# Performance work log

Hardware: AMD Instinct MI355X
Metric: run time of the kernel (lower is better)

Reference implementation:

```python
import jax, jax.numpy as jnp
import numpy as np

HIDDEN = 1024
N_HEADS = 16
HEAD_DIM = HIDDEN // N_HEADS


def apply_rope(x, freqs):
    # x: [b, s, h, d]; freqs: [s, d//2]
    b, s, h, d = x.shape
    x2 = x.reshape(b, s, h, d // 2, 2)
    x_real, x_imag = x2[..., 0], x2[..., 1]
    cos = jnp.cos(freqs)[None, :, None, :]  # [1, s, 1, d//2]
    sin = jnp.sin(freqs)[None, :, None, :]
    out_real = x_real * cos - x_imag * sin
    out_imag = x_real * sin + x_imag * cos
    return jnp.stack([out_real, out_imag], axis=-1).reshape(b, s, h, d)


def setup_inputs() -> dict:
    key = jax.random.key(0)
    k_x, k_f, k_wq, k_bq, k_wo, k_bo = jax.random.split(key, 6)
    b, s = 2, 2048
    x = jax.random.normal(k_x, (b, s, HIDDEN), dtype=jnp.float32)
    freqs = jax.random.normal(k_f, (s, HEAD_DIM // 2), dtype=jnp.float32)
    lim = 1.0 / np.sqrt(HIDDEN)
    W_qkv = jax.random.uniform(k_wq, (HIDDEN, 3 * HIDDEN), jnp.float32, -lim, lim)
    b_qkv = jax.random.uniform(k_bq, (3 * HIDDEN,), jnp.float32, -lim, lim)
    W_out = jax.random.uniform(k_wo, (HIDDEN, HIDDEN), jnp.float32, -lim, lim)
    b_out = jax.random.uniform(k_bo, (HIDDEN,), jnp.float32, -lim, lim)
    return {"x": x, "freqs": freqs, "W_qkv": W_qkv, "b_qkv": b_qkv,
            "W_out": W_out, "b_out": b_out}


def reference(x, freqs, W_qkv, b_qkv, W_out, b_out):
    b, s, c = x.shape
    h, d = N_HEADS, HEAD_DIM
    qkv = jnp.einsum('bsc,cf->bsf', x, W_qkv) + b_qkv  # [b, s, 3*c]
    qkv = qkv.reshape(b, s, 3, h, d)
    q, k, v = qkv[:, :, 0], qkv[:, :, 1], qkv[:, :, 2]  # [b, s, h, d]
    q = apply_rope(q, freqs)
    k = apply_rope(k, freqs)
    scale = 1.0 / np.sqrt(d).astype(np.float32)
    scores = jnp.einsum('bqhd,bkhd->bhqk', q, k) * scale  # [b, h, s, s]
    attn = jax.nn.softmax(scores, axis=-1)
    out = jnp.einsum('bhqk,bkhd->bqhd', attn, v).reshape(b, s, c)
    return jnp.einsum('bsc,cf->bsf', out, W_out) + b_out
```

## Files before the change

kernel.cpp:

```cpp
#include <hip/hip_runtime.h>
#include <math.h>

constexpr int kB = 2;
constexpr int kS = 2048;
constexpr int kC = 1024;
constexpr int kH = 16;
constexpr int kD = 64;
constexpr int kF = 3072;
constexpr int kT = kB * kS;

typedef __attribute__((ext_vector_type(8))) short short8v;
typedef __attribute__((ext_vector_type(4))) short short4v;
typedef __attribute__((ext_vector_type(4))) float f32x4;
typedef __attribute__((ext_vector_type(16))) float f32x16;

__device__ __forceinline__ short f2bf(float f) {
    unsigned u = __builtin_bit_cast(unsigned, f);
    u += 0x7fffu + ((u >> 16) & 1u);
    return (short)(u >> 16);
}

__device__ __forceinline__ unsigned cvtpk(float a, float b) {
    unsigned r;
    asm("v_cvt_pk_bf16_f32 %0, %1, %2" : "=v"(r) : "v"(a), "v"(b));
    return r;
}

__device__ __forceinline__ unsigned pk_bf16(float a, float b) {
    unsigned ua = __builtin_bit_cast(unsigned, a);
    ua += 0x7fffu + ((ua >> 16) & 1u);
    unsigned ub = __builtin_bit_cast(unsigned, b);
    ub += 0x7fffu + ((ub >> 16) & 1u);
    return (ua >> 16) | (ub & 0xffff0000u);
}

__device__ __forceinline__ void gl_lds16(const void* g, void* l) {
    __builtin_amdgcn_global_load_lds(
        (const __attribute__((address_space(1))) char*)g,
        (__attribute__((address_space(3))) char*)l, 16, 0, 0);
}

__device__ __forceinline__ f32x4 mfma16(short8v a, short8v b, f32x4 c) {
    return __builtin_amdgcn_mfma_f32_16x16x32_bf16(a, b, c, 0, 0, 0);
}
__device__ __forceinline__ f32x16 mfma32(short8v a, short8v b, f32x16 c) {
    return __builtin_amdgcn_mfma_f32_32x32x16_bf16(a, b, c, 0, 0, 0);
}

__device__ __forceinline__ void tcvt_body(const float* __restrict__ w,
                                          short* __restrict__ wt, int K, int N,
                                          int bx, int by, int t, float Ts[64][65]) {
    const int n0 = bx * 64, k0 = by * 64;
    const int r = t >> 4, c4 = (t & 15) * 4;
#pragma unroll
    for (int rr = 0; rr < 64; rr += 16) {
        float4 v = *reinterpret_cast<const float4*>(&w[(size_t)(k0 + r + rr) * N + n0 + c4]);
        Ts[r + rr][c4 + 0] = v.x; Ts[r + rr][c4 + 1] = v.y;
        Ts[r + rr][c4 + 2] = v.z; Ts[r + rr][c4 + 3] = v.w;
    }
    __syncthreads();
#pragma unroll
    for (int rr = 0; rr < 64; rr += 16) {
        int n = r + rr;
        short4v o = { f2bf(Ts[c4 + 0][n]), f2bf(Ts[c4 + 1][n]),
                      f2bf(Ts[c4 + 2][n]), f2bf(Ts[c4 + 3][n]) };
        *reinterpret_cast<short4v*>(&wt[(size_t)(n0 + n) * K + k0 + c4]) = o;
    }
}

__global__ __launch_bounds__(256) void prep_kernel(
    const float* __restrict__ x, short* __restrict__ xb,
    const float* __restrict__ wq, short* __restrict__ wqt,
    const float* __restrict__ wo, short* __restrict__ wot,
    const float* __restrict__ freqs, float* __restrict__ cost,
    float* __restrict__ sint) {
    __shared__ float Ts[64][65];
    const int bid = blockIdx.x, t = threadIdx.x;
    if (bid < 4096) {
        int i = bid * 256 + t;
        float4 v = reinterpret_cast<const float4*>(x)[i];
        short4v o = { f2bf(v.x), f2bf(v.y), f2bf(v.z), f2bf(v.w) };
        reinterpret_cast<short4v*>(xb)[i] = o;
    } else if (bid < 4864) {
        int i = bid - 4096;
        tcvt_body(wq, wqt, kC, kF, i % 48, i / 48, t, Ts);
    } else if (bid < 5120) {
        int i = bid - 4864;
        tcvt_body(wo, wot, kC, kC, i % 16, i / 16, t, Ts);
    } else {
        int i = (bid - 5120) * 256 + t;
        float f = freqs[i];
        float s, c;
        sincosf(f, &s, &c);
        cost[i] = c; sint[i] = s;
    }
}

__device__ __forceinline__ void gemm_main(const short* __restrict__ A,
                                          const short* __restrict__ Bt,
                                          int m0, int n0, short* Als, short* Bls,
                                          f32x4 acc[4][4]) {
    const int tid = threadIdx.x, wid = tid >> 6, lane = tid & 63;
    const int srow = lane >> 3, schunk = lane & 7;
    const int fr = lane & 15, fg = lane >> 4;
    const int wm = (wid >> 1) * 64, wn = (wid & 1) * 64;
    for (int kt = 0; kt < 1024; kt += 64) {
        __syncthreads();
#pragma unroll
        for (int j = 0; j < 4; ++j) {
            int i = wid * 4 + j;
            int row = i * 8 + srow;
            gl_lds16(&A[(size_t)(m0 + row) * 1024 + kt + ((schunk ^ (row & 7)) << 3)],
                     &Als[i * 512]);
        }
#pragma unroll
        for (int j = 0; j < 4; ++j) {
            int i = wid * 4 + j;
            int row = i * 8 + srow;
            gl_lds16(&Bt[(size_t)(n0 + row) * 1024 + kt + ((schunk ^ (row & 7)) << 3)],
                     &Bls[i * 512]);
        }
        __syncthreads();
#pragma unroll
        for (int kk = 0; kk < 2; ++kk) {
            short8v af[4], bf[4];
#pragma unroll
            for (int fm = 0; fm < 4; ++fm) {
                int row = wm + fm * 16 + fr;
                af[fm] = *reinterpret_cast<const short8v*>(
                    &Als[row * 64 + (((fg + 4 * kk) ^ (row & 7)) << 3)]);
            }
#pragma unroll
            for (int fn = 0; fn < 4; ++fn) {
                int row = wn + fn * 16 + fr;
                bf[fn] = *reinterpret_cast<const short8v*>(
                    &Bls[row * 64 + (((fg + 4 * kk) ^ (row & 7)) << 3)]);
            }
#pragma unroll
            for (int fm = 0; fm < 4; ++fm)
#pragma unroll
                for (int fn = 0; fn < 4; ++fn)
                    acc[fm][fn] = mfma16(af[fm], bf[fn], acc[fm][fn]);
        }
    }
}

__global__ __launch_bounds__(256) void qkv_gemm_kernel(
    const short* __restrict__ xb, const short* __restrict__ wqt,
    const float* __restrict__ bias, const float* __restrict__ cost,
    const float* __restrict__ sint,
    short* __restrict__ qg, short* __restrict__ kg, short* __restrict__ vt) {
    __shared__ __attribute__((aligned(16))) short Als[128 * 64];
    __shared__ __attribute__((aligned(16))) short Bls[128 * 64];
    f32x4 acc[4][4] = {};
    const int tid = threadIdx.x, wid = tid >> 6, lane = tid & 63;
    const int m0 = blockIdx.y * 128, n0 = blockIdx.x * 128;
    gemm_main(xb, wqt, m0, n0, Als, Bls, acc);

    const int fr = lane & 15, fg = lane >> 4;
    const int wm = (wid >> 1) * 64, wn = (wid & 1) * 64;
    const int which = (n0 + wn) >> 10;
    const int bidx = m0 >> 11;
#pragma unroll
    for (int fn = 0; fn < 4; ++fn) {
        int col = n0 + wn + fn * 16 + fr;
        float bv = bias[col];
        int d = col & 63;
        int h = (col >> 6) & 15;
        int p0 = d >> 1;
        int odd = d & 1;
#pragma unroll
        for (int fm = 0; fm < 4; ++fm) {
            int r0 = m0 + wm + fm * 16 + fg * 4;
            int s0 = r0 & 2047;
            float c[4];
#pragma unroll
            for (int r = 0; r < 4; ++r) c[r] = acc[fm][fn][r] + bv;
            if (which < 2) {
#pragma unroll
                for (int r = 0; r < 4; ++r) {
                    float cs = cost[(s0 + r) * 32 + p0];
                    float sn = sint[(s0 + r) * 32 + p0];
                    float p = __shfl_xor(c[r], 1);
                    float o = odd ? fmaf(p, sn, c[r] * cs) : fmaf(-p, sn, c[r] * cs);
                    c[r] = (which == 0) ? o * 0.1803368801f : o;
                }
                short* dst = which ? kg : qg;
                size_t base = ((size_t)(bidx * 16 + h) * 2048 + s0) * 64 + d;
#pragma unroll
                for (int r = 0; r < 4; ++r) dst[base + (size_t)r * 64] = f2bf(c[r]);
            } else {
                short4v o = { f2bf(c[0]), f2bf(c[1]), f2bf(c[2]), f2bf(c[3]) };
                *reinterpret_cast<short4v*>(
                    &vt[((size_t)(bidx * 16 + h) * 64 + d) * 2048 + s0]) = o;
            }
        }
    }
}

__global__ __launch_bounds__(256, 3) void attn_mfma_kernel(
    const short* __restrict__ qg, const short* __restrict__ kg,
    const short* __restrict__ vt, short* __restrict__ ab) {
    __shared__ __attribute__((aligned(16))) short LDSBUF[3 * 8192];
    const int tid = threadIdx.x, wid = tid >> 6, lane = tid & 63;
    const int l31 = lane & 31, hi = lane >> 5;
    const int p = wid >> 1;
    const int wq = wid & 1;
    const int r8 = lane >> 3, c8 = lane & 7;
    const int soff = 8 * (c8 ^ r8);

    const int bid = blockIdx.x;
    const int swz = (bid & 7) * 128 + (bid >> 3);
    const int bh = swz >> 5;
    const int q0 = (swz & 31) * 64 + wq * 32;

    const short* qb = qg + (size_t)bh * 2048 * 64;
    const short* kb = kg + (size_t)bh * 2048 * 64;
    const short* vb = vt + (size_t)bh * 64 * 2048;

    short8v qf[4];
#pragma unroll
    for (int kkq = 0; kkq < 4; ++kkq)
        qf[kkq] = *reinterpret_cast<const short8v*>(
            &qb[(size_t)(q0 + l31) * 64 + kkq * 16 + hi * 8]);

    f32x16 o[2] = {};
    float l_i = 0.f;

    auto stage = [&](int t, short* buf) {
        const int kt = t * 32;
        short* Kd = buf + p * 2048 + (wq * 8) * 64;
        const short* Ks = kb + (size_t)(p * 1024 + kt) * 64;
#pragma unroll
        for (int j = 0; j < 2; ++j) {
            int row = j * 16 + wq * 8 + r8;
            gl_lds16(Ks + (size_t)row * 64 + soff, Kd + j * 1024);
        }
        short* Vd = buf + 4096 + (wid * 8) * 64;
        const int s = c8 ^ r8;
#pragma unroll
        for (int j = 0; j < 2; ++j) {
            int d = j * 32 + wid * 8 + r8;
            gl_lds16(vb + (size_t)d * 2048 + (s >> 2) * 1024 + kt + (s & 3) * 8,
                     Vd + j * 2048);
        }
    };

    stage(0, LDSBUF);
    stage(1, LDSBUF + 8192);

    for (int t = 0; t < 32; ++t) {
        __builtin_amdgcn_sched_barrier(0);
        if (t < 31) {
            asm volatile("s_waitcnt vmcnt(4)" ::: "memory");
        } else {
            asm volatile("s_waitcnt vmcnt(0)" ::: "memory");
        }
        __builtin_amdgcn_s_barrier();
        __builtin_amdgcn_sched_barrier(0);

        short* bufc = LDSBUF + (t % 3) * 8192;
        if (t + 2 < 32) stage(t + 2, LDSBUF + ((t + 2) % 3) * 8192);

        const short* Kb = bufc + p * 2048;
        const short* Vb = bufc + 4096;

        f32x16 sacc = {};
#pragma unroll
        for (int kkq = 0; kkq < 4; ++kkq) {
            short8v a = *reinterpret_cast<const short8v*>(
                &Kb[l31 * 64 + (((kkq * 2 + hi) ^ (l31 & 7)) << 3)]);
            sacc = mfma32(a, qf[kkq], sacc);
        }

#pragma unroll
        for (int r = 0; r < 16; ++r) sacc[r] = __builtin_amdgcn_exp2f(sacc[r]);
        float t8[8];
#pragma unroll
        for (int r = 0; r < 8; ++r) t8[r] = sacc[r] + sacc[r + 8];
        float t4[4];
#pragma unroll
        for (int r = 0; r < 4; ++r) t4[r] = t8[r] + t8[r + 4];
        float rs = (t4[0] + t4[1]) + (t4[2] + t4[3]);
        rs += __shfl_xor(rs, 32);
        l_i += rs;

        unsigned c[8];
#pragma unroll
        for (int i = 0; i < 8; ++i) c[i] = cvtpk(sacc[2 * i], sacc[2 * i + 1]);
        short8v pb[2];
#pragma unroll
        for (int kk = 0; kk < 2; ++kk) {
            unsigned a0 = c[kk * 4 + 0], a1 = c[kk * 4 + 1];
            unsigned a2 = c[kk * 4 + 2], a3 = c[kk * 4 + 3];
            unsigned s0x = (unsigned)__shfl_xor((int)a0, 32);
            unsigned s1x = (unsigned)__shfl_xor((int)a1, 32);
            unsigned s2x = (unsigned)__shfl_xor((int)a2, 32);
            unsigned s3x = (unsigned)__shfl_xor((int)a3, 32);
            uint4 w;
            w.x = hi ? s2x : a0;
            w.y = hi ? s3x : a1;
            w.z = hi ? a2 : s0x;
            w.w = hi ? a3 : s1x;
            pb[kk] = __builtin_bit_cast(short8v, w);
        }

#pragma unroll
        for (int kk = 0; kk < 2; ++kk) {
            short8v v0 = *reinterpret_cast<const short8v*>(
                &Vb[l31 * 64 + (((p * 4 + kk * 2 + hi) ^ (l31 & 7)) << 3)]);
            short8v v1 = *reinterpret_cast<const short8v*>(
                &Vb[(32 + l31) * 64 + (((p * 4 + kk * 2 + hi) ^ (l31 & 7)) << 3)]);
            o[0] = mfma32(v0, pb[kk], o[0]);
            o[1] = mfma32(v1, pb[kk], o[1]);
        }
    }

    __syncthreads();

    float* olds = reinterpret_cast<float*>(LDSBUF + 4096);
    float* lls  = olds + 2 * 2304;
    if (p == 1) {
        float* ob = olds + wq * 2304 + lane * 36;
#pragma unroll
        for (int i = 0; i < 4; ++i) {
            f32x4 w0 = { o[0][4 * i + 0], o[0][4 * i + 1], o[0][4 * i + 2], o[0][4 * i + 3] };
            *reinterpret_cast<f32x4*>(ob + i * 4) = w0;
            f32x4 w1 = { o[1][4 * i + 0], o[1][4 * i + 1], o[1][4 * i + 2], o[1][4 * i + 3] };
            *reinterpret_cast<f32x4*>(ob + 16 + i * 4) = w1;
        }
        lls[wq * 64 + lane] = l_i;
    }
    __syncthreads();
    if (p == 0) {
        float* ob = olds + wq * 2304 + lane * 36;
#pragma unroll
        for (int i = 0; i < 4; ++i) {
            f32x4 w0 = *reinterpret_cast<const f32x4*>(ob + i * 4);
            f32x4 w1 = *reinterpret_cast<const f32x4*>(ob + 16 + i * 4);
#pragma unroll
            for (int j = 0; j < 4; ++j) {
                o[0][4 * i + j] += w0[j];
                o[1][4 * i + j] += w1[j];
            }
        }
        l_i += lls[wq * 64 + lane];

        const float inv = 1.f / l_i;
        short* ep = LDSBUF + wid * 2048;
        const int q = l31;
#pragma unroll
        for (int fd = 0; fd < 2; ++fd)
#pragma unroll
            for (int i = 0; i < 4; ++i) {
                int d0 = fd * 32 + 8 * i + 4 * hi;
                uint2 w;
                w.x = pk_bf16(o[fd][4 * i + 0] * inv, o[fd][4 * i + 1] * inv);
                w.y = pk_bf16(o[fd][4 * i + 2] * inv, o[fd][4 * i + 3] * inv);
                *reinterpret_cast<uint2*>(&ep[q * 64 + (d0 ^ (8 * (q & 3)))]) = w;
            }
        __builtin_amdgcn_s_waitcnt(0);
        const int bb = bh >> 4, hh = bh & 15;
        const int wrow = r8, wcol = c8;
#pragma unroll
        for (int j = 0; j < 4; ++j) {
            int row = j * 8 + wrow;
            short8v tv = *reinterpret_cast<const short8v*>(
                &ep[row * 64 + ((8 * wcol) ^ (8 * (row & 3)))]);
            int s = q0 + row;
            *reinterpret_cast<short8v*>(
                &ab[(size_t)(bb * 2048 + s) * 1024 + hh * 64 + 8 * wcol]) = tv;
        }
    }
}

__global__ __launch_bounds__(256) void out_gemm_kernel(
    const short* __restrict__ ab, const short* __restrict__ wot,
    const float* __restrict__ bias, float* __restrict__ out) {
    __shared__ __attribute__((aligned(16))) short Als[128 * 64];
    __shared__ __attribute__((aligned(16))) short Bls[128 * 64];
    f32x4 acc[4][4] = {};
    const int tid = threadIdx.x, wid = tid >> 6, lane = tid & 63;
    const int m0 = blockIdx.y * 128, n0 = blockIdx.x * 128;
    gemm_main(ab, wot, m0, n0, Als, Bls, acc);
    const int fr = lane & 15, fg = lane >> 4;
    const int wm = (wid >> 1) * 64, wn = (wid & 1) * 64;
#pragma unroll
    for (int fn = 0; fn < 4; ++fn) {
        int col = n0 + wn + fn * 16 + fr;
        float bv = bias[col];
#pragma unroll
        for (int fm = 0; fm < 4; ++fm) {
            int r0 = m0 + wm + fm * 16 + fg * 4;
#pragma unroll
            for (int r = 0; r < 4; ++r)
                out[(size_t)(r0 + r) * 1024 + col] = acc[fm][fn][r] + bv;
        }
    }
}

extern "C" void kernel_launch(void* const* d_in, const int* in_sizes, int n_in,
                              void* d_out, int out_size, void* d_ws, size_t ws_size,
                              hipStream_t stream) {
    const float* x     = (const float*)d_in[0];
    const float* freqs = (const float*)d_in[1];
    const float* W_qkv = (const float*)d_in[2];
    const float* b_qkv = (const float*)d_in[3];
    const float* W_out = (const float*)d_in[4];
    const float* b_out = (const float*)d_in[5];
    float* out = (float*)d_out;

    char* w = (char*)d_ws;
    short* xb  = (short*)w;  w += (size_t)kT * kC * 2;
    short* wqt = (short*)w;  w += (size_t)kF * kC * 2;
    short* wot = (short*)w;  w += (size_t)kC * kC * 2;
    short* qgw = (short*)w;  w += (size_t)kB * kH * kS * kD * 2;
    short* kgw = (short*)w;  w += (size_t)kB * kH * kS * kD * 2;
    short* vtw = (short*)w;  w += (size_t)kB * kH * kS * kD * 2;
    short* abw = (short*)w;  w += (size_t)kT * kC * 2;
    float* costt = (float*)w; w += (size_t)kS * (kD / 2) * 4;
    float* sintt = (float*)w; w += (size_t)kS * (kD / 2) * 4;

    prep_kernel<<<dim3(5376), 256, 0, stream>>>(x, xb, W_qkv, wqt, W_out, wot,
                                                freqs, costt, sintt);
    qkv_gemm_kernel<<<dim3(kF / 128, kT / 128), 256, 0, stream>>>(
        xb, wqt, b_qkv, costt, sintt, qgw, kgw, vtw);
    attn_mfma_kernel<<<dim3(1024), 256, 0, stream>>>(qgw, kgw, vtw, abw);
    out_gemm_kernel<<<dim3(kC / 128, kT / 128), 256, 0, stream>>>(abw, wot, b_out, out);
}
```

Before: 137.0 us.

## Restructure attention kernel: each wave covers 64 queries over a key quarter

```diff
diff --git a/kernel.cpp b/kernel.cpp
--- a/kernel.cpp
+++ b/kernel.cpp
@@ -24,6 +24,10 @@
     unsigned r;
     asm("v_cvt_pk_bf16_f32 %0, %1, %2" : "=v"(r) : "v"(a), "v"(b));
     return r;
+}
+
+__device__ __forceinline__ void plane32_swap(unsigned& a, unsigned& b) {
+    asm volatile("v_permlane32_swap_b32 %0, %1" : "+v"(a), "+v"(b));
 }
 
 __device__ __forceinline__ unsigned pk_bf16(float a, float b) {
@@ -201,176 +205,148 @@
 __global__ __launch_bounds__(256, 3) void attn_mfma_kernel(
     const short* __restrict__ qg, const short* __restrict__ kg,
     const short* __restrict__ vt, short* __restrict__ ab) {
-    __shared__ __attribute__((aligned(16))) short LDSBUF[3 * 8192];
+    __shared__ __attribute__((aligned(16))) short LDSBUF[16384];
+    short* Kls = LDSBUF;
+    short* Vls = LDSBUF + 8192;
     const int tid = threadIdx.x, wid = tid >> 6, lane = tid & 63;
     const int l31 = lane & 31, hi = lane >> 5;
-    const int p = wid >> 1;
-    const int wq = wid & 1;
     const int r8 = lane >> 3, c8 = lane & 7;
-    const int soff = 8 * (c8 ^ r8);
 
     const int bid = blockIdx.x;
     const int swz = (bid & 7) * 128 + (bid >> 3);
     const int bh = swz >> 5;
-    const int q0 = (swz & 31) * 64 + wq * 32;
+    const int q0 = (swz & 31) * 64;
 
     const short* qb = qg + (size_t)bh * 2048 * 64;
     const short* kb = kg + (size_t)bh * 2048 * 64;
     const short* vb = vt + (size_t)bh * 64 * 2048;
 
-    short8v qf[4];
-#pragma unroll
-    for (int kkq = 0; kkq < 4; ++kkq)
-        qf[kkq] = *reinterpret_cast<const short8v*>(
-            &qb[(size_t)(q0 + l31) * 64 + kkq * 16 + hi * 8]);
-
-    f32x16 o[2] = {};
-    float l_i = 0.f;
-
-    auto stage = [&](int t, short* buf) {
-        const int kt = t * 32;
-        short* Kd = buf + p * 2048 + (wq * 8) * 64;
-        const short* Ks = kb + (size_t)(p * 1024 + kt) * 64;
-#pragma unroll
-        for (int j = 0; j < 2; ++j) {
-            int row = j * 16 + wq * 8 + r8;
-            gl_lds16(Ks + (size_t)row * 64 + soff, Kd + j * 1024);
-        }
-        short* Vd = buf + 4096 + (wid * 8) * 64;
-        const int s = c8 ^ r8;
-#pragma unroll
-        for (int j = 0; j < 2; ++j) {
-            int d = j * 32 + wid * 8 + r8;
-            gl_lds16(vb + (size_t)d * 2048 + (s >> 2) * 1024 + kt + (s & 3) * 8,
-                     Vd + j * 2048);
-        }
-    };
-
-    stage(0, LDSBUF);
-    stage(1, LDSBUF + 8192);
-
-    for (int t = 0; t < 32; ++t) {
-        __builtin_amdgcn_sched_barrier(0);
-        if (t < 31) {
-            asm volatile("s_waitcnt vmcnt(4)" ::: "memory");
-        } else {
-            asm volatile("s_waitcnt vmcnt(0)" ::: "memory");
-        }
-        __builtin_amdgcn_s_barrier();
-        __builtin_amdgcn_sched_barrier(0);
-
-        short* bufc = LDSBUF + (t % 3) * 8192;
-        if (t + 2 < 32) stage(t + 2, LDSBUF + ((t + 2) % 3) * 8192);
-
-        const short* Kb = bufc + p * 2048;
-        const short* Vb = bufc + 4096;
-
-        f32x16 sacc = {};
+    short8v qf[2][4];
+#pragma unroll
+    for (int qt = 0; qt < 2; ++qt)
+#pragma unroll
+        for (int kkq = 0; kkq < 4; ++kkq)
+            qf[qt][kkq] = *reinterpret_cast<const short8v*>(
+                &qb[(size_t)(q0 + qt * 32 + l31) * 64 + kkq * 16 + hi * 8]);
+
+    f32x16 o[2][2] = {};
+    float l_loc[2] = {0.f, 0.f};
+
+    const int soffK = 8 * (c8 ^ r8);
+
+    for (int t = 0; t < 16; ++t) {
+        const int kt = t * 128;
+        __syncthreads();
+#pragma unroll
+        for (int j = 0; j < 4; ++j)
+            gl_lds16(kb + (size_t)(kt + wid * 32 + j * 8 + r8) * 64 + soffK,
+                     Kls + (wid * 32 + j * 8) * 64);
+#pragma unroll
+        for (int j = 0; j < 4; ++j) {
+            int d = wid * 16 + j * 4 + (lane >> 4);
+            int c = lane & 15;
+            gl_lds16(vb + (size_t)d * 2048 + kt + ((c ^ (d & 15)) * 8),
+                     Vls + (wid * 16 + j * 4) * 128);
+        }
+        __syncthreads();
+
+        f32x16 sacc[2] = {};
 #pragma unroll
         for (int kkq = 0; kkq < 4; ++kkq) {
-            short8v a = *reinterpret_cast<const short8v*>(
-                &Kb[l31 * 64 + (((kkq * 2 + hi) ^ (l31 & 7)) << 3)]);
-            sacc = mfma32(a, qf[kkq], sacc);
-        }
-
-#pragma unroll
-        for (int r = 0; r < 16; ++r) sacc[r] = __builtin_amdgcn_exp2f(sacc[r]);
-        float t8[8];
-#pragma unroll
-        for (int r = 0; r < 8; ++r) t8[r] = sacc[r] + sacc[r + 8];
-        float t4[4];
-#pragma unroll
-        for (int r = 0; r < 4; ++r) t4[r] = t8[r] + t8[r + 4];
-        float rs = (t4[0] + t4[1]) + (t4[2] + t4[3]);
-        rs += __shfl_xor(rs, 32);
-        l_i += rs;
-
-        unsigned c[8];
-#pragma unroll
-        for (int i = 0; i < 8; ++i) c[i] = cvtpk(sacc[2 * i], sacc[2 * i + 1]);
-        short8v pb[2];
-#pragma unroll
-        for (int kk = 0; kk < 2; ++kk) {
-            unsigned a0 = c[kk * 4 + 0], a1 = c[kk * 4 + 1];
-            unsigned a2 = c[kk * 4 + 2], a3 = c[kk * 4 + 3];
-            unsigned s0x = (unsigned)__shfl_xor((int)a0, 32);
-            unsigned s1x = (unsigned)__shfl_xor((int)a1, 32);
-            unsigned s2x = (unsigned)__shfl_xor((int)a2, 32);
-            unsigned s3x = (unsigned)__shfl_xor((int)a3, 32);
-            uint4 w;
-            w.x = hi ? s2x : a0;
-            w.y = hi ? s3x : a1;
-            w.z = hi ? a2 : s0x;
-            w.w = hi ? a3 : s1x;
-            pb[kk] = __builtin_bit_cast(short8v, w);
-        }
-
-#pragma unroll
-        for (int kk = 0; kk < 2; ++kk) {
-            short8v v0 = *reinterpret_cast<const short8v*>(
-                &Vb[l31 * 64 + (((p * 4 + kk * 2 + hi) ^ (l31 & 7)) << 3)]);
-            short8v v1 = *reinterpret_cast<const short8v*>(
-                &Vb[(32 + l31) * 64 + (((p * 4 + kk * 2 + hi) ^ (l31 & 7)) << 3)]);
-            o[0] = mfma32(v0, pb[kk], o[0]);
-            o[1] = mfma32(v1, pb[kk], o[1]);
-        }
+            short8v kf = *reinterpret_cast<const short8v*>(
+                &Kls[(wid * 32 + l31) * 64 + (((kkq * 2 + hi) ^ (l31 & 7)) << 3)]);
+            sacc[0] = mfma32(kf, qf[0][kkq], sacc[0]);
+            sacc[1] = mfma32(kf, qf[1][kkq], sacc[1]);
+        }
+
+        short8v pb[2][2];
+#pragma unroll
+        for (int qt = 0; qt < 2; ++qt) {
+#pragma unroll
+            for (int r = 0; r < 16; ++r)
+                sacc[qt][r] = __builtin_amdgcn_exp2f(sacc[qt][r]);
+            float t8[8];
+#pragma unroll
+            for (int r = 0; r < 8; ++r) t8[r] = sacc[qt][r] + sacc[qt][r + 8];
+            float t4[4];
+#pragma unroll
+            for (int r = 0; r < 4; ++r) t4[r] = t8[r] + t8[r + 4];
+            l_loc[qt] += (t4[0] + t4[1]) + (t4[2] + t4[3]);
+            unsigned c[4][2];
+#pragma unroll
+            for (int g = 0; g < 4; ++g) {
+                c[g][0] = cvtpk(sacc[qt][g * 4 + 0], sacc[qt][g * 4 + 1]);
+                c[g][1] = cvtpk(sacc[qt][g * 4 + 2], sacc[qt][g * 4 + 3]);
+            }
+#pragma unroll
+            for (int kk = 0; kk < 2; ++kk) {
+                unsigned x0 = c[2 * kk][0], y0 = c[2 * kk + 1][0];
+                unsigned x1 = c[2 * kk][1], y1 = c[2 * kk + 1][1];
+                plane32_swap(x0, y0);
+                plane32_swap(x1, y1);
+                uint4 w;
+                w.x = x0; w.y = x1; w.z = y0; w.w = y1;
+                pb[qt][kk] = __builtin_bit_cast(short8v, w);
+            }
+        }
+
+#pragma unroll
+        for (int kk = 0; kk < 2; ++kk)
+#pragma unroll
+            for (int fd = 0; fd < 2; ++fd) {
+                int d = fd * 32 + l31;
+                short8v vf = *reinterpret_cast<const short8v*>(
+                    &Vls[d * 128 + (((wid * 4 + kk * 2 + hi) ^ (d & 15)) << 3)]);
+                o[fd][0] = mfma32(vf, pb[0][kk], o[fd][0]);
+                o[fd][1] = mfma32(vf, pb[1][kk], o[fd][1]);
+            }
     }
 
     __syncthreads();
 
-    float* olds = reinterpret_cast<float*>(LDSBUF + 4096);
-    float* lls  = olds + 2 * 2304;
-    if (p == 1) {
-        float* ob = olds + wq * 2304 + lane * 36;
-#pragma unroll
-        for (int i = 0; i < 4; ++i) {
-            f32x4 w0 = { o[0][4 * i + 0], o[0][4 * i + 1], o[0][4 * i + 2], o[0][4 * i + 3] };
-            *reinterpret_cast<f32x4*>(ob + i * 4) = w0;
-            f32x4 w1 = { o[1][4 * i + 0], o[1][4 * i + 1], o[1][4 * i + 2], o[1][4 * i + 3] };
-            *reinterpret_cast<f32x4*>(ob + 16 + i * 4) = w1;
-        }
-        lls[wq * 64 + lane] = l_i;
-    }
-    __syncthreads();
-    if (p == 0) {
-        float* ob = olds + wq * 2304 + lane * 36;
-#pragma unroll
-        for (int i = 0; i < 4; ++i) {
-            f32x4 w0 = *reinterpret_cast<const f32x4*>(ob + i * 4);
-            f32x4 w1 = *reinterpret_cast<const f32x4*>(ob + 16 + i * 4);
-#pragma unroll
-            for (int j = 0; j < 4; ++j) {
-                o[0][4 * i + j] += w0[j];
-                o[1][4 * i + j] += w1[j];
-            }
-        }
-        l_i += lls[wq * 64 + lane];
-
-        const float inv = 1.f / l_i;
-        short* ep = LDSBUF + wid * 2048;
-        const int q = l31;
-#pragma unroll
-        for (int fd = 0; fd < 2; ++fd)
-#pragma unroll
-            for (int i = 0; i < 4; ++i) {
-                int d0 = fd * 32 + 8 * i + 4 * hi;
-                uint2 w;
-                w.x = pk_bf16(o[fd][4 * i + 0] * inv, o[fd][4 * i + 1] * inv);
-                w.y = pk_bf16(o[fd][4 * i + 2] * inv, o[fd][4 * i + 3] * inv);
-                *reinterpret_cast<uint2*>(&ep[q * 64 + (d0 ^ (8 * (q & 3)))]) = w;
-            }
-        __builtin_amdgcn_s_waitcnt(0);
+    float* Oacc = reinterpret_cast<float*>(LDSBUF);
+    float* lacc = Oacc + 64 * 65;
+    float l2[2];
+#pragma unroll
+    for (int qt = 0; qt < 2; ++qt)
+        l2[qt] = l_loc[qt] + __shfl_xor(l_loc[qt], 32);
+    for (int w = 0; w < 4; ++w) {
+        if (wid == w) {
+#pragma unroll
+            for (int qt = 0; qt < 2; ++qt) {
+                int q = qt * 32 + l31;
+#pragma unroll
+                for (int fd = 0; fd < 2; ++fd)
+#pragma unroll
+                    for (int r = 0; r < 16; ++r) {
+                        int d = fd * 32 + (r & 3) + 8 * (r >> 2) + 4 * hi;
+                        if (w == 0) Oacc[q * 65 + d] = o[fd][qt][r];
+                        else        Oacc[q * 65 + d] += o[fd][qt][r];
+                    }
+                if (hi == 0) {
+                    if (w == 0) lacc[q] = l2[qt];
+                    else        lacc[q] += l2[qt];
+                }
+            }
+        }
+        __syncthreads();
+    }
+    {
+        const int q = tid >> 2, dc = (tid & 3) * 16;
+        const float inv = 1.f / lacc[q];
+        unsigned u[8];
+#pragma unroll
+        for (int i = 0; i < 8; ++i) {
+            float a = Oacc[q * 65 + dc + 2 * i] * inv;
+            float b = Oacc[q * 65 + dc + 2 * i + 1] * inv;
+            u[i] = pk_bf16(a, b);
+        }
         const int bb = bh >> 4, hh = bh & 15;
-        const int wrow = r8, wcol = c8;
-#pragma unroll
-        for (int j = 0; j < 4; ++j) {
-            int row = j * 8 + wrow;
-            short8v tv = *reinterpret_cast<const short8v*>(
-                &ep[row * 64 + ((8 * wcol) ^ (8 * (row & 3)))]);
-            int s = q0 + row;
-            *reinterpret_cast<short8v*>(
-                &ab[(size_t)(bb * 2048 + s) * 1024 + hh * 64 + 8 * wcol]) = tv;
-        }
+        size_t base = (size_t)(bb * 2048 + q0 + q) * 1024 + hh * 64 + dc;
+        uint4 w0; w0.x = u[0]; w0.y = u[1]; w0.z = u[2]; w0.w = u[3];
+        uint4 w1; w1.x = u[4]; w1.y = u[5]; w1.z = u[6]; w1.w = u[7];
+        *reinterpret_cast<uint4*>(&ab[base]) = w0;
+        *reinterpret_cast<uint4*>(&ab[base + 8]) = w1;
     }
 }
 
```

Measured after the change: 135.5 us. Within noise of the previous version (-1.1%).

## Retile QKV GEMM to 256x256 with 4-stage LDS ring; double-buffer attention

Applied to the files above, without the earlier changes.

```diff
diff --git a/kernel.cpp b/kernel.cpp
--- a/kernel.cpp
+++ b/kernel.cpp
@@ -96,6 +96,127 @@
     }
 }
 
+__global__ __launch_bounds__(512, 2) void qkv_gemm_kernel(
+    const short* __restrict__ xb, const short* __restrict__ wqt,
+    const float* __restrict__ bias, const float* __restrict__ cost,
+    const float* __restrict__ sint,
+    short* __restrict__ qg, short* __restrict__ kg, short* __restrict__ vt) {
+    __shared__ __attribute__((aligned(16))) short Als[4][8192];
+    __shared__ __attribute__((aligned(16))) short Bls[4][8192];
+    const int tid = threadIdx.x, wid = tid >> 6, lane = tid & 63;
+    const int fr = lane & 15, fg = lane >> 4;
+    const int wr = wid >> 2, wc = wid & 3;
+
+    const int bid = blockIdx.x;
+    const int swz = (bid & 7) * 24 + (bid >> 3);
+    const int m0 = (swz / 12) * 256, n0 = (swz % 12) * 256;
+
+    auto stageKT = [&](int ktile) {
+        const int buf = ktile & 3;
+        const int kt = ktile * 32;
+#pragma unroll
+        for (int j = 0; j < 2; ++j) {
+            int flat = wid * 128 + j * 64 + lane;
+            int row = flat >> 2, c = flat & 3;
+            gl_lds16(&xb[(size_t)(m0 + row) * 1024 + kt + ((c ^ (row & 3)) << 3)],
+                     &Als[buf][flat * 8]);
+        }
+#pragma unroll
+        for (int j = 0; j < 2; ++j) {
+            int flat = wid * 128 + j * 64 + lane;
+            int row = flat >> 2, c = flat & 3;
+            gl_lds16(&wqt[(size_t)(n0 + row) * 1024 + kt + ((c ^ (row & 3)) << 3)],
+                     &Bls[buf][flat * 8]);
+        }
+    };
+
+    f32x4 acc[8][4] = {};
+    stageKT(0);
+    stageKT(1);
+
+    for (int k = 0; k < 32; ++k) {
+        const int buf = k & 3;
+        __builtin_amdgcn_sched_barrier(0);
+        if (k < 31) {
+            asm volatile("s_waitcnt vmcnt(4)" ::: "memory");
+        } else {
+            asm volatile("s_waitcnt vmcnt(0)" ::: "memory");
+        }
+        __builtin_amdgcn_s_barrier();
+        __builtin_amdgcn_sched_barrier(0);
+        if (k + 2 < 32) stageKT(k + 2);
+
+        short8v bf[4], af[4];
+#pragma unroll
+        for (int fn = 0; fn < 4; ++fn) {
+            int row = wc * 64 + fn * 16 + fr;
+            bf[fn] = *reinterpret_cast<const short8v*>(
+                &Bls[buf][(row * 4 + (fg ^ (row & 3))) * 8]);
+        }
+#pragma unroll
+        for (int fm = 0; fm < 4; ++fm) {
+            int row = wr * 128 + fm * 16 + fr;
+            af[fm] = *reinterpret_cast<const short8v*>(
+                &Als[buf][(row * 4 + (fg ^ (row & 3))) * 8]);
+        }
+#pragma unroll
+        for (int fm = 0; fm < 4; ++fm)
+#pragma unroll
+            for (int fn = 0; fn < 4; ++fn)
+                acc[fm][fn] = mfma16(af[fm], bf[fn], acc[fm][fn]);
+#pragma unroll
+        for (int fm = 0; fm < 4; ++fm) {
+            int row = wr * 128 + (fm + 4) * 16 + fr;
+            af[fm] = *reinterpret_cast<const short8v*>(
+                &Als[buf][(row * 4 + (fg ^ (row & 3))) * 8]);
+        }
+#pragma unroll
+        for (int fm = 0; fm < 4; ++fm)
+#pragma unroll
+            for (int fn = 0; fn < 4; ++fn)
+                acc[fm + 4][fn] = mfma16(af[fm], bf[fn], acc[fm + 4][fn]);
+    }
+
+    const int col_base = n0 + wc * 64;
+    const int which = col_base >> 10;
+    const int bidx = m0 >> 11;
+#pragma unroll
+    for (int fn = 0; fn < 4; ++fn) {
+        int col = col_base + fn * 16 + fr;
+        float bv = bias[col];
+        int d = col & 63;
+        int h = (col >> 6) & 15;
+        int p0 = d >> 1;
+        int odd = d & 1;
+#pragma unroll
+        for (int fm = 0; fm < 8; ++fm) {
+            int r0 = m0 + wr * 128 + fm * 16 + fg * 4;
+            int s0 = r0 & 2047;
+            float c[4];
+#pragma unroll
+            for (int r = 0; r < 4; ++r) c[r] = acc[fm][fn][r] + bv;
+            if (which < 2) {
+#pragma unroll
+                for (int r = 0; r < 4; ++r) {
+                    float cs = cost[(s0 + r) * 32 + p0];
+                    float sn = sint[(s0 + r) * 32 + p0];
+                    float p = __shfl_xor(c[r], 1);
+                    float o = odd ? fmaf(p, sn, c[r] * cs) : fmaf(-p, sn, c[r] * cs);
+                    c[r] = (which == 0) ? o * 0.1803368801f : o;
+                }
+                short* dst = which ? kg : qg;
+                size_t base = ((size_t)(bidx * 16 + h) * 2048 + s0) * 64 + d;
+#pragma unroll
+                for (int r = 0; r < 4; ++r) dst[base + (size_t)r * 64] = f2bf(c[r]);
+            } else {
+                short4v o = { f2bf(c[0]), f2bf(c[1]), f2bf(c[2]), f2bf(c[3]) };
+                *reinterpret_cast<short4v*>(
+                    &vt[((size_t)(bidx * 16 + h) * 64 + d) * 2048 + s0]) = o;
+            }
+        }
+    }
+}
+
 __device__ __forceinline__ void gemm_main(const short* __restrict__ A,
                                           const short* __restrict__ Bt,
                                           int m0, int n0, short* Als, short* Bls,
@@ -145,63 +266,10 @@
     }
 }
 
-__global__ __launch_bounds__(256) void qkv_gemm_kernel(
-    const short* __restrict__ xb, const short* __restrict__ wqt,
-    const float* __restrict__ bias, const float* __restrict__ cost,
-    const float* __restrict__ sint,
-    short* __restrict__ qg, short* __restrict__ kg, short* __restrict__ vt) {
-    __shared__ __attribute__((aligned(16))) short Als[128 * 64];
-    __shared__ __attribute__((aligned(16))) short Bls[128 * 64];
-    f32x4 acc[4][4] = {};
-    const int tid = threadIdx.x, wid = tid >> 6, lane = tid & 63;
-    const int m0 = blockIdx.y * 128, n0 = blockIdx.x * 128;
-    gemm_main(xb, wqt, m0, n0, Als, Bls, acc);
-
-    const int fr = lane & 15, fg = lane >> 4;
-    const int wm = (wid >> 1) * 64, wn = (wid & 1) * 64;
-    const int which = (n0 + wn) >> 10;
-    const int bidx = m0 >> 11;
-#pragma unroll
-    for (int fn = 0; fn < 4; ++fn) {
-        int col = n0 + wn + fn * 16 + fr;
-        float bv = bias[col];
-        int d = col & 63;
-        int h = (col >> 6) & 15;
-        int p0 = d >> 1;
-        int odd = d & 1;
-#pragma unroll
-        for (int fm = 0; fm < 4; ++fm) {
-            int r0 = m0 + wm + fm * 16 + fg * 4;
-            int s0 = r0 & 2047;
-            float c[4];
-#pragma unroll
-            for (int r = 0; r < 4; ++r) c[r] = acc[fm][fn][r] + bv;
-            if (which < 2) {
-#pragma unroll
-                for (int r = 0; r < 4; ++r) {
-                    float cs = cost[(s0 + r) * 32 + p0];
-                    float sn = sint[(s0 + r) * 32 + p0];
-                    float p = __shfl_xor(c[r], 1);
-                    float o = odd ? fmaf(p, sn, c[r] * cs) : fmaf(-p, sn, c[r] * cs);
-                    c[r] = (which == 0) ? o * 0.1803368801f : o;
-                }
-                short* dst = which ? kg : qg;
-                size_t base = ((size_t)(bidx * 16 + h) * 2048 + s0) * 64 + d;
-#pragma unroll
-                for (int r = 0; r < 4; ++r) dst[base + (size_t)r * 64] = f2bf(c[r]);
-            } else {
-                short4v o = { f2bf(c[0]), f2bf(c[1]), f2bf(c[2]), f2bf(c[3]) };
-                *reinterpret_cast<short4v*>(
-                    &vt[((size_t)(bidx * 16 + h) * 64 + d) * 2048 + s0]) = o;
-            }
-        }
-    }
-}
-
-__global__ __launch_bounds__(256, 3) void attn_mfma_kernel(
+__global__ __launch_bounds__(256, 4) void attn_mfma_kernel(
     const short* __restrict__ qg, const short* __restrict__ kg,
     const short* __restrict__ vt, short* __restrict__ ab) {
-    __shared__ __attribute__((aligned(16))) short LDSBUF[3 * 8192];
+    __shared__ __attribute__((aligned(16))) short LDSBUF[16384];
     const int tid = threadIdx.x, wid = tid >> 6, lane = tid & 63;
     const int l31 = lane & 31, hi = lane >> 5;
     const int p = wid >> 1;
@@ -227,16 +295,16 @@
     f32x16 o[2] = {};
     float l_i = 0.f;
 
-    auto stage = [&](int t, short* buf) {
+    auto stage = [&](int t, int buf) {
         const int kt = t * 32;
-        short* Kd = buf + p * 2048 + (wq * 8) * 64;
+        short* Kd = LDSBUF + buf * 8192 + p * 2048 + (wq * 8) * 64;
         const short* Ks = kb + (size_t)(p * 1024 + kt) * 64;
 #pragma unroll
         for (int j = 0; j < 2; ++j) {
             int row = j * 16 + wq * 8 + r8;
             gl_lds16(Ks + (size_t)row * 64 + soff, Kd + j * 1024);
         }
-        short* Vd = buf + 4096 + (wid * 8) * 64;
+        short* Vd = LDSBUF + buf * 8192 + 4096 + (wid * 8) * 64;
         const int s = c8 ^ r8;
 #pragma unroll
         for (int j = 0; j < 2; ++j) {
@@ -246,24 +314,14 @@
         }
     };
 
-    stage(0, LDSBUF);
-    stage(1, LDSBUF + 8192);
+    stage(0, 0);
+    __syncthreads();
 
     for (int t = 0; t < 32; ++t) {
-        __builtin_amdgcn_sched_barrier(0);
-        if (t < 31) {
-            asm volatile("s_waitcnt vmcnt(4)" ::: "memory");
-        } else {
-            asm volatile("s_waitcnt vmcnt(0)" ::: "memory");
-        }
-        __builtin_amdgcn_s_barrier();
-        __builtin_amdgcn_sched_barrier(0);
-
-        short* bufc = LDSBUF + (t % 3) * 8192;
-        if (t + 2 < 32) stage(t + 2, LDSBUF + ((t + 2) % 3) * 8192);
-
-        const short* Kb = bufc + p * 2048;
-        const short* Vb = bufc + 4096;
+        const int buf = t & 1;
+        if (t + 1 < 32) stage(t + 1, buf ^ 1);
+        const short* Kb = LDSBUF + buf * 8192 + p * 2048;
+        const short* Vb = LDSBUF + buf * 8192 + 4096;
 
         f32x16 sacc = {};
 #pragma unroll
@@ -314,9 +372,8 @@
             o[0] = mfma32(v0, pb[kk], o[0]);
             o[1] = mfma32(v1, pb[kk], o[1]);
         }
-    }
-
-    __syncthreads();
+        __syncthreads();
+    }
 
     float* olds = reinterpret_cast<float*>(LDSBUF + 4096);
     float* lls  = olds + 2 * 2304;
@@ -423,7 +480,7 @@
 
     prep_kernel<<<dim3(5376), 256, 0, stream>>>(x, xb, W_qkv, wqt, W_out, wot,
                                                 freqs, costt, sintt);
-    qkv_gemm_kernel<<<dim3(kF / 128, kT / 128), 256, 0, stream>>>(
+    qkv_gemm_kernel<<<dim3(192), 512, 0, stream>>>(
         xb, wqt, b_qkv, costt, sintt, qgw, kgw, vtw);
     attn_mfma_kernel<<<dim3(1024), 256, 0, stream>>>(qgw, kgw, vtw, abw);
     out_gemm_kernel<<<dim3(kC / 128, kT / 128), 256, 0, stream>>>(abw, wot, b_out, out);
```

Result: slower. 145.5 us (+6.2%).
